# Optimization experiments

Hardware: AMD Instinct MI355X
Metric: run time of the kernel (lower is better)

## Reference

```python
import jax, jax.numpy as jnp
import numpy as np

S = 1024      # MAX_SEQ_LEN
D_IN = 4096
H = 32        # num_heads
G = 8         # num_kv_groups
HD = 128      # head_dim
GS = H // G   # group_size


def _rope(t, cos, sin):
    # t: [heads, S, HD]; cos/sin: [S, HD]
    half = HD // 2
    t1, t2 = t[..., :half], t[..., half:]
    rotated = jnp.concatenate([-t2, t1], axis=-1)
    return t * cos[None] + rotated * sin[None]


def setup_inputs() -> dict:
    key = jax.random.key(0)
    ks = jax.random.split(key, 8)
    x = jax.random.normal(ks[0], (1, S, D_IN), dtype=jnp.float32)
    mask = jnp.triu(jnp.ones((S, S), dtype=bool), k=1)  # causal: True above diagonal
    # RoPE tables (standard llama frequencies)
    inv_freq = 1.0 / (10000.0 ** (jnp.arange(0, HD, 2, dtype=jnp.float32) / HD))
    angles = jnp.arange(S, dtype=jnp.float32)[:, None] * inv_freq[None, :]  # [S, HD/2]
    angles = jnp.concatenate([angles, angles], axis=-1)                     # [S, HD]
    cos, sin = jnp.cos(angles), jnp.sin(angles)
    sc = 0.02
    Wq = jax.random.normal(ks[1], (D_IN, H * HD), dtype=jnp.float32) * sc
    Wk = jax.random.normal(ks[2], (D_IN, G * HD), dtype=jnp.float32) * sc
    Wv = jax.random.normal(ks[3], (D_IN, G * HD), dtype=jnp.float32) * sc
    Wo = jax.random.normal(ks[4], (H * HD, D_IN), dtype=jnp.float32) * sc
    return {"x": x, "mask": mask, "cos": cos, "sin": sin,
            "Wq": Wq, "Wk": Wk, "Wv": Wv, "Wo": Wo}


def reference(x, mask, cos, sin, Wq, Wk, Wv, Wo):
    b, n_tok, _ = x.shape  # b == 1 (module squeezes dim 0)
    xs = x[0]                                        # [S, d_in]
    q = (xs @ Wq).reshape(n_tok, H, HD).transpose(1, 0, 2)   # [H, S, HD]
    k = (xs @ Wk).reshape(n_tok, G, HD).transpose(1, 0, 2)   # [G, S, HD]
    v = (xs @ Wv).reshape(n_tok, G, HD).transpose(1, 0, 2)   # [G, S, HD]
    q = _rope(q, cos, sin)
    k = _rope(k, cos, sin)
    # GQA expansion: repeat_interleave over head dim
    k = jnp.repeat(k, GS, axis=0)                    # [H, S, HD]
    v = jnp.repeat(v, GS, axis=0)
    scores = jnp.einsum('hsd,htd->hst', q, k)        # [H, S, S]
    scores = jnp.where(mask[None], -jnp.inf, scores) / jnp.sqrt(jnp.float32(HD))
    weights = jax.nn.softmax(scores, axis=-1)
    ctx = jnp.einsum('hst,htd->hsd', weights, v)     # [H, S, HD]
    ctx = ctx.transpose(1, 0, 2).reshape(n_tok, H * HD)
    out = ctx @ Wo                                   # [S, d_in]
    return out[None]                                 # [1, S, d_in]
```

## Files before the change

kernel.cpp:

```cpp
#include <hip/hip_runtime.h>
#include <hip/hip_bf16.h>

#define S_LEN 1024
#define DIN 4096
#define NH 32
#define NG 8
#define HD 128

typedef __bf16 bf16x8 __attribute__((ext_vector_type(8)));
typedef __bf16 bf16x4 __attribute__((ext_vector_type(4)));
typedef float f32x4 __attribute__((ext_vector_type(4)));

__device__ __forceinline__ void gload_lds16(const void* g, void* l) {
  __builtin_amdgcn_global_load_lds(
      (const __attribute__((address_space(1))) unsigned int*)g,
      (__attribute__((address_space(3))) unsigned int*)l, 16, 0, 0);
}

__device__ __forceinline__ unsigned pack2bf(float a, float b) {
  union { __bf16 h[2]; unsigned u; } x;
  x.h[0] = (__bf16)a; x.h[1] = (__bf16)b;
  return x.u;
}

__global__ __launch_bounds__(256) void k_prep(const float* __restrict__ x,
                                              const float* __restrict__ Wq,
                                              const float* __restrict__ Wk,
                                              const float* __restrict__ Wv,
                                              const float* __restrict__ Wo,
                                              __bf16* __restrict__ xb,
                                              __bf16* __restrict__ WqkvT,
                                              __bf16* __restrict__ WoT) {
  __shared__ unsigned t3[32 * 256];
  const int tid = threadIdx.x;
  int bid = blockIdx.x;
  if (bid < 4096) {
    int i = bid * 256 + tid;
    const float4 v = ((const float4*)x)[i];
    bf16x4 o;
    o.x = (__bf16)v.x; o.y = (__bf16)v.y; o.z = (__bf16)v.z; o.w = (__bf16)v.w;
    ((bf16x4*)xb)[i] = o;
    return;
  }
  bid -= 4096;
  const int nt = bid % 40, kt = bid / 40;
  const int k0 = kt * 64;
  const float* W; __bf16* WT; int N, nsrc0, nd0;
  if (nt < 16)       { W = Wq; WT = WqkvT; N = 4096; nsrc0 = nt * 256;        nd0 = nt * 256; }
  else if (nt < 20)  { W = Wk; WT = WqkvT; N = 1024; nsrc0 = (nt - 16) * 256; nd0 = 4096 + (nt - 16) * 256; }
  else if (nt < 24)  { W = Wv; WT = WqkvT; N = 1024; nsrc0 = (nt - 20) * 256; nd0 = 5120 + (nt - 20) * 256; }
  else               { W = Wo; WT = WoT;   N = 4096; nsrc0 = (nt - 24) * 256; nd0 = (nt - 24) * 256; }

#pragma unroll
  for (int p = 0; p < 8; ++p) {
    int s = p * 256 + tid;
    int kp = s >> 6;
    int nq = s & 63;
    const float* src = &W[(size_t)(k0 + 2 * kp) * N + nsrc0 + 4 * nq];
    const float4 a = *(const float4*)src;
    const float4 b = *(const float4*)(src + N);
    int cphys = nq ^ ((kp >> 1) & 7);
    uint4 d;
    d.x = pack2bf(a.x, b.x);
    d.y = pack2bf(a.y, b.y);
    d.z = pack2bf(a.z, b.z);
    d.w = pack2bf(a.w, b.w);
    *(uint4*)&t3[kp * 256 + cphys * 4] = d;
  }
  __syncthreads();

#pragma unroll
  for (int it = 0; it < 8; ++it) {
    int n = it * 32 + (tid >> 3);
    int u = tid & 7;
    int nq = n >> 2, j = n & 3;
    uint4 d;
    d.x = t3[(4 * u + 0) * 256 + ((nq ^ (((4 * u + 0) >> 1) & 7)) << 2) + j];
    d.y = t3[(4 * u + 1) * 256 + ((nq ^ (((4 * u + 1) >> 1) & 7)) << 2) + j];
    d.z = t3[(4 * u + 2) * 256 + ((nq ^ (((4 * u + 2) >> 1) & 7)) << 2) + j];
    d.w = t3[(4 * u + 3) * 256 + ((nq ^ (((4 * u + 3) >> 1) & 7)) << 2) + j];
    *(uint4*)&WT[(size_t)(nd0 + n) * DIN + k0 + 8 * u] = d;
  }
}

__global__ __launch_bounds__(256) void k_rope(__bf16* __restrict__ Q, __bf16* __restrict__ Kb,
                                              const float* __restrict__ cosT,
                                              const float* __restrict__ sinT) {
  int idx = blockIdx.x * 256 + threadIdx.x;
  int d = (idx & 15) * 4;
  int row = idx >> 4;
  __bf16* p; int s;
  if (row < S_LEN * NH) { p = Q + (size_t)row * HD; s = row >> 5; }
  else { int r = row - S_LEN * NH; p = Kb + (size_t)r * HD; s = r >> 3; }
  const float4 c = *(const float4*)&cosT[s * HD + d];
  const float4 sn = *(const float4*)&sinT[s * HD + d];
  bf16x4 a = *(const bf16x4*)&p[d];
  bf16x4 b = *(const bf16x4*)&p[d + 64];
  bf16x4 oa, ob;
  oa.x = (__bf16)((float)a.x * c.x - (float)b.x * sn.x);
  oa.y = (__bf16)((float)a.y * c.y - (float)b.y * sn.y);
  oa.z = (__bf16)((float)a.z * c.z - (float)b.z * sn.z);
  oa.w = (__bf16)((float)a.w * c.w - (float)b.w * sn.w);
  ob.x = (__bf16)((float)b.x * c.x + (float)a.x * sn.x);
  ob.y = (__bf16)((float)b.y * c.y + (float)a.y * sn.y);
  ob.z = (__bf16)((float)b.z * c.z + (float)a.z * sn.z);
  ob.w = (__bf16)((float)b.w * c.w + (float)a.w * sn.w);
  *(bf16x4*)&p[d] = oa;
  *(bf16x4*)&p[d + 64] = ob;
}

template <int MODE>
__global__ __launch_bounds__(256, 3) void k_gemm(const __bf16* __restrict__ A,
                                                 const __bf16* __restrict__ Bt,
                                                 float* __restrict__ C,
                                                 __bf16* __restrict__ Qb,
                                                 __bf16* __restrict__ Kb,
                                                 __bf16* __restrict__ Vt) {
  __shared__ __bf16 As[2][128 * 64];
  __shared__ __bf16 Bs[2][64 * 64];
  const int bm = blockIdx.y, bn = blockIdx.x;
  const int K = DIN, NT = K / 64;

  const int tid = threadIdx.x, w = tid >> 6;
  const int l = tid & 63, l15 = l & 15, g4 = l >> 4;

  const __bf16* Asrc = A + (size_t)(bm * 128) * K;
  const __bf16* Bsrc = Bt + (size_t)(bn * 64) * K;

  f32x4 acc[2][4];
#pragma unroll
  for (int i = 0; i < 2; ++i)
#pragma unroll
    for (int j = 0; j < 4; ++j)
#pragma unroll
      for (int r = 0; r < 4; ++r) acc[i][j][r] = 0.f;

  auto issueA = [&](int t, __bf16* dst) {
#pragma unroll
    for (int p = 0; p < 4; ++p) {
      int c = p * 256 + tid;
      int row = c >> 3, gc = (c & 7) ^ (row & 7);
      gload_lds16(Asrc + (size_t)row * K + t * 64 + gc * 8, dst + (p * 256 + w * 64) * 8);
    }
  };
  auto issueB = [&](int t, __bf16* dst) {
#pragma unroll
    for (int p = 0; p < 2; ++p) {
      int c = p * 256 + tid;
      int row = c >> 3, gc = (c & 7) ^ (row & 7);
      gload_lds16(Bsrc + (size_t)row * K + t * 64 + gc * 8, dst + (p * 256 + w * 64) * 8);
    }
  };
  auto compute = [&](const __bf16* Ab, const __bf16* Bb) {
    bf16x8 af[2][2], bfr[4][2];
#pragma unroll
    for (int i = 0; i < 2; ++i) {
      int m = w * 32 + i * 16 + l15;
#pragma unroll
      for (int kk = 0; kk < 2; ++kk)
        af[i][kk] = *(const bf16x8*)((const char*)Ab + m * 128 + (((kk * 4 + g4) ^ (m & 7)) << 4));
    }
#pragma unroll
    for (int j = 0; j < 4; ++j) {
      int n = j * 16 + l15;
#pragma unroll
      for (int kk = 0; kk < 2; ++kk)
        bfr[j][kk] = *(const bf16x8*)((const char*)Bb + n * 128 + (((kk * 4 + g4) ^ (n & 7)) << 4));
    }
#pragma unroll
    for (int kk = 0; kk < 2; ++kk)
#pragma unroll
      for (int i = 0; i < 2; ++i)
#pragma unroll
        for (int j = 0; j < 4; ++j)
          acc[i][j] = __builtin_amdgcn_mfma_f32_16x16x32_bf16(af[i][kk], bfr[j][kk], acc[i][j], 0, 0, 0);
  };

  issueA(0, As[0]); issueB(0, Bs[0]);
  __syncthreads();

  for (int t = 0; t < NT; t += 2) {
    issueA(t + 1, As[1]); issueB(t + 1, Bs[1]);
    compute(As[0], Bs[0]);
    __syncthreads();
    if (t + 2 < NT) { issueA(t + 2, As[0]); issueB(t + 2, Bs[0]); }
    compute(As[1], Bs[1]);
    __syncthreads();
  }

  if constexpr (MODE == 0) {
#pragma unroll
    for (int i = 0; i < 2; ++i)
#pragma unroll
      for (int j = 0; j < 4; ++j)
#pragma unroll
        for (int r = 0; r < 4; ++r) {
          size_t row = bm * 128 + w * 32 + i * 16 + g4 * 4 + r;
          size_t col = bn * 64 + j * 16 + l15;
          C[row * 4096 + col] = acc[i][j][r];
        }
  } else {
    const int nb0 = bn * 64;
    if (bn < 80) {
      __bf16* dst = (bn < 64) ? Qb : Kb;
      int ldc = (bn < 64) ? 4096 : 1024;
      int coff = (bn < 64) ? 0 : 4096;
#pragma unroll
      for (int i = 0; i < 2; ++i)
#pragma unroll
        for (int j = 0; j < 4; ++j)
#pragma unroll
          for (int r = 0; r < 4; ++r) {
            size_t row = bm * 128 + w * 32 + i * 16 + g4 * 4 + r;
            size_t col = nb0 - coff + j * 16 + l15;
            dst[row * ldc + col] = (__bf16)acc[i][j][r];
          }
    } else {
#pragma unroll
      for (int i = 0; i < 2; ++i)
#pragma unroll
        for (int j = 0; j < 4; ++j) {
          size_t n = nb0 - 5120 + j * 16 + l15;
          size_t m0 = bm * 128 + w * 32 + i * 16 + g4 * 4;
          bf16x4 v;
          v.x = (__bf16)acc[i][j][0]; v.y = (__bf16)acc[i][j][1];
          v.z = (__bf16)acc[i][j][2]; v.w = (__bf16)acc[i][j][3];
          *(bf16x4*)&Vt[n * 1024 + m0] = v;
        }
    }
  }
}

__global__ __launch_bounds__(256) void k_attn(const __bf16* __restrict__ Q,
                                              const __bf16* __restrict__ Kb,
                                              const __bf16* __restrict__ Vt,
                                              __bf16* __restrict__ ctx) {
  __shared__ __align__(16) char lds_raw[65536];
  __bf16* Ks = (__bf16*)lds_raw;
  __bf16* Vs = (__bf16*)(lds_raw + 32768);

  const int h = blockIdx.y, g = h >> 2;
  const int q0 = blockIdx.x * 64;
  const int tid = threadIdx.x, w = tid >> 6, l = tid & 63;
  const int l15 = l & 15, g4 = l >> 4;
  const float scale = 0.08838834764831845f;

  bf16x8 qf[4];
  const int qrow = q0 + w * 16 + l15;
#pragma unroll
  for (int ks = 0; ks < 4; ++ks)
    qf[ks] = *(const bf16x8*)&Q[(size_t)qrow * (NH * HD) + h * HD + ks * 32 + g4 * 8];

  f32x4 acc[8];
#pragma unroll
  for (int i = 0; i < 8; ++i)
#pragma unroll
    for (int r = 0; r < 4; ++r) acc[i][r] = 0.f;
  float m_run = -__builtin_inff(), l_run = 0.f;

  const int ntiles = (q0 + 64 + 127) >> 7;
  for (int kt = 0; kt < ntiles; ++kt) {
    const int kv0 = kt * 128;
#pragma unroll
    for (int p = 0; p < 8; ++p) {
      int c = p * 256 + tid;
      int row = c >> 4, cc = c & 15;
      gload_lds16(&Kb[(size_t)(kv0 + row) * (NG * HD) + g * HD + ((cc ^ (row & 7)) << 3)],
                  &Ks[(p * 256 + w * 64) * 8]);
      gload_lds16(&Vt[(size_t)(g * HD + row) * S_LEN + kv0 + ((cc ^ (row & 7)) << 3)],
                  &Vs[(p * 256 + w * 64) * 8]);
    }
    __syncthreads();

    float sreg[8][4];
    const bool need_mask = (kv0 + 127 > q0);
#pragma unroll
    for (int tf = 0; tf < 8; ++tf) {
      f32x4 sa;
#pragma unroll
      for (int r = 0; r < 4; ++r) sa[r] = 0.f;
      int t_loc = tf * 16 + l15;
#pragma unroll
      for (int ks = 0; ks < 4; ++ks) {
        bf16x8 kf = *(const bf16x8*)((const char*)Ks + t_loc * 256 + (((ks * 4 + g4) ^ (t_loc & 7)) << 4));
        sa = __builtin_amdgcn_mfma_f32_16x16x32_bf16(kf, qf[ks], sa, 0, 0, 0);
      }
#pragma unroll
      for (int r = 0; r < 4; ++r) {
        float v = sa[r] * scale;
        if (need_mask && (kv0 + tf * 16 + g4 * 4 + r) > qrow) v = -__builtin_inff();
        sreg[tf][r] = v;
      }
    }
    float mx = -__builtin_inff();
#pragma unroll
    for (int tf = 0; tf < 8; ++tf)
#pragma unroll
      for (int r = 0; r < 4; ++r) mx = fmaxf(mx, sreg[tf][r]);
    mx = fmaxf(mx, __shfl_xor(mx, 16));
    mx = fmaxf(mx, __shfl_xor(mx, 32));
    const float m_new = fmaxf(m_run, mx);
    const float alpha = __expf(m_run - m_new);
    float ssum = 0.f;
#pragma unroll
    for (int tf = 0; tf < 8; ++tf)
#pragma unroll
      for (int r = 0; r < 4; ++r) {
        sreg[tf][r] = __expf(sreg[tf][r] - m_new);
        ssum += sreg[tf][r];
      }
    ssum += __shfl_xor(ssum, 16);
    ssum += __shfl_xor(ssum, 32);
    l_run = l_run * alpha + ssum;
    m_run = m_new;
    float ar[4];
#pragma unroll
    for (int r = 0; r < 4; ++r) ar[r] = __shfl(alpha, g4 * 4 + r);
#pragma unroll
    for (int nf = 0; nf < 8; ++nf)
#pragma unroll
      for (int r = 0; r < 4; ++r) acc[nf][r] *= ar[r];

    __syncthreads();

    char* pb = lds_raw + w * 4096;
#pragma unroll
    for (int tf = 0; tf < 8; ++tf) {
      int chunkc = 2 * tf + (g4 >> 1);
      int addr = l15 * 256 + ((chunkc ^ (l15 & 7)) << 4) + ((g4 & 1) << 3);
      *(unsigned*)(pb + addr)     = pack2bf(sreg[tf][0], sreg[tf][1]);
      *(unsigned*)(pb + addr + 4) = pack2bf(sreg[tf][2], sreg[tf][3]);
    }
    asm volatile("s_waitcnt lgkmcnt(0)" ::: "memory");
    bf16x8 pf[4];
#pragma unroll
    for (int ks = 0; ks < 4; ++ks)
      pf[ks] = *(const bf16x8*)(pb + l15 * 256 + (((ks * 4 + g4) ^ (l15 & 7)) << 4));
#pragma unroll
    for (int nf = 0; nf < 8; ++nf) {
      int d_loc = nf * 16 + l15;
#pragma unroll
      for (int ks = 0; ks < 4; ++ks) {
        bf16x8 vf = *(const bf16x8*)((const char*)Vs + d_loc * 256 + (((ks * 4 + g4) ^ (d_loc & 7)) << 4));
        acc[nf] = __builtin_amdgcn_mfma_f32_16x16x32_bf16(pf[ks], vf, acc[nf], 0, 0, 0);
      }
    }
    __syncthreads();
  }
  float li[4];
#pragma unroll
  for (int r = 0; r < 4; ++r) li[r] = 1.f / __shfl(l_run, g4 * 4 + r);
#pragma unroll
  for (int nf = 0; nf < 8; ++nf)
#pragma unroll
    for (int r = 0; r < 4; ++r) {
      size_t row = q0 + w * 16 + g4 * 4 + r;
      size_t col = (size_t)h * HD + nf * 16 + l15;
      ctx[row * (NH * HD) + col] = (__bf16)(acc[nf][r] * li[r]);
    }
}

extern "C" void kernel_launch(void* const* d_in, const int* in_sizes, int n_in,
                              void* d_out, int out_size, void* d_ws, size_t ws_size,
                              hipStream_t stream) {
  const float* x    = (const float*)d_in[0];
  const float* cosT = (const float*)d_in[2];
  const float* sinT = (const float*)d_in[3];
  const float* Wq   = (const float*)d_in[4];
  const float* Wk   = (const float*)d_in[5];
  const float* Wv   = (const float*)d_in[6];
  const float* Wo   = (const float*)d_in[7];
  float* out = (float*)d_out;

  char* ws = (char*)d_ws;
  const size_t MB = 1u << 20;
  __bf16* xb    = (__bf16*)(ws + 0);
  __bf16* WqkvT = (__bf16*)(ws + 8 * MB);
  __bf16* WoT   = (__bf16*)(ws + 56 * MB);
  __bf16* Qb    = (__bf16*)(ws + 88 * MB);
  __bf16* Kbuf  = (__bf16*)(ws + 96 * MB);
  __bf16* Vtb   = (__bf16*)(ws + 98 * MB);
  __bf16* ctxb  = (__bf16*)(ws + 0);

  k_prep<<<4096 + 2560, 256, 0, stream>>>(x, Wq, Wk, Wv, Wo, xb, WqkvT, WoT);

  k_gemm<1><<<dim3(96, 8), 256, 0, stream>>>(xb, WqkvT, nullptr, Qb, Kbuf, Vtb);

  k_rope<<<2560, 256, 0, stream>>>(Qb, Kbuf, cosT, sinT);

  k_attn<<<dim3(16, 32), 256, 0, stream>>>(Qb, Kbuf, Vtb, ctxb);

  k_gemm<0><<<dim3(64, 8), 256, 0, stream>>>(ctxb, WoT, out, nullptr, nullptr, nullptr);
}
```

Measured before the change: 214.9 us.

## Pre-tile transposed weights into contiguous pre-swizzled 64x64 blocks for B loads

The weight-conversion kernel now writes the transposed bf16 weights as contiguous 64x64 tiles, with the XOR swizzle already applied, ordered by N-tile then K-tile. The GEMM's B loader then reads each K-step tile as one contiguous 8 KB chunk instead of 64 rows strided by the full K. This removes per-row address arithmetic and makes the B global loads fully sequential. It depends on the GEMM consuming the same tile order, which the new Bsrc and issueB indexing provide.

```diff
diff --git a/kernel.cpp b/kernel.cpp
--- a/kernel.cpp
+++ b/kernel.cpp
@@ -45,11 +45,11 @@
   bid -= 4096;
   const int nt = bid % 40, kt = bid / 40;
   const int k0 = kt * 64;
-  const float* W; __bf16* WT; int N, nsrc0, nd0;
-  if (nt < 16)       { W = Wq; WT = WqkvT; N = 4096; nsrc0 = nt * 256;        nd0 = nt * 256; }
-  else if (nt < 20)  { W = Wk; WT = WqkvT; N = 1024; nsrc0 = (nt - 16) * 256; nd0 = 4096 + (nt - 16) * 256; }
-  else if (nt < 24)  { W = Wv; WT = WqkvT; N = 1024; nsrc0 = (nt - 20) * 256; nd0 = 5120 + (nt - 20) * 256; }
-  else               { W = Wo; WT = WoT;   N = 4096; nsrc0 = (nt - 24) * 256; nd0 = (nt - 24) * 256; }
+  const float* W; __bf16* WT; int N, nsrc0, tn0;
+  if (nt < 16)       { W = Wq; WT = WqkvT; N = 4096; nsrc0 = nt * 256;        tn0 = nt * 4; }
+  else if (nt < 20)  { W = Wk; WT = WqkvT; N = 1024; nsrc0 = (nt - 16) * 256; tn0 = 64 + (nt - 16) * 4; }
+  else if (nt < 24)  { W = Wv; WT = WqkvT; N = 1024; nsrc0 = (nt - 20) * 256; tn0 = 80 + (nt - 20) * 4; }
+  else               { W = Wo; WT = WoT;   N = 4096; nsrc0 = (nt - 24) * 256; tn0 = (nt - 24) * 4; }
 
 #pragma unroll
   for (int p = 0; p < 8; ++p) {
@@ -71,15 +71,20 @@
 
 #pragma unroll
   for (int it = 0; it < 8; ++it) {
-    int n = it * 32 + (tid >> 3);
-    int u = tid & 7;
+    int slot = it * 256 + tid;
+    int ts = slot >> 9;
+    int c = slot & 511;
+    int row = c >> 3;
+    int lc = (c & 7) ^ (row & 7);
+    int n = ts * 64 + row;
     int nq = n >> 2, j = n & 3;
+    int kp0 = 4 * lc;
     uint4 d;
-    d.x = t3[(4 * u + 0) * 256 + ((nq ^ (((4 * u + 0) >> 1) & 7)) << 2) + j];
-    d.y = t3[(4 * u + 1) * 256 + ((nq ^ (((4 * u + 1) >> 1) & 7)) << 2) + j];
-    d.z = t3[(4 * u + 2) * 256 + ((nq ^ (((4 * u + 2) >> 1) & 7)) << 2) + j];
-    d.w = t3[(4 * u + 3) * 256 + ((nq ^ (((4 * u + 3) >> 1) & 7)) << 2) + j];
-    *(uint4*)&WT[(size_t)(nd0 + n) * DIN + k0 + 8 * u] = d;
+    d.x = t3[(kp0 + 0) * 256 + ((nq ^ (((kp0 + 0) >> 1) & 7)) << 2) + j];
+    d.y = t3[(kp0 + 1) * 256 + ((nq ^ (((kp0 + 1) >> 1) & 7)) << 2) + j];
+    d.z = t3[(kp0 + 2) * 256 + ((nq ^ (((kp0 + 2) >> 1) & 7)) << 2) + j];
+    d.w = t3[(kp0 + 3) * 256 + ((nq ^ (((kp0 + 3) >> 1) & 7)) << 2) + j];
+    *(uint4*)&WT[(((size_t)tn0 + ts) * 64 + kt) * 4096 + (size_t)c * 8] = d;
   }
 }
 
@@ -125,7 +130,7 @@
   const int l = tid & 63, l15 = l & 15, g4 = l >> 4;
 
   const __bf16* Asrc = A + (size_t)(bm * 128) * K;
-  const __bf16* Bsrc = Bt + (size_t)(bn * 64) * K;
+  const __bf16* Bsrc = Bt + (size_t)bn * 64 * 4096;
 
   f32x4 acc[2][4];
 #pragma unroll
@@ -144,11 +149,11 @@
     }
   };
   auto issueB = [&](int t, __bf16* dst) {
+    const __bf16* tile = Bsrc + (size_t)t * 4096;
 #pragma unroll
     for (int p = 0; p < 2; ++p) {
       int c = p * 256 + tid;
-      int row = c >> 3, gc = (c & 7) ^ (row & 7);
-      gload_lds16(Bsrc + (size_t)row * K + t * 64 + gc * 8, dst + (p * 256 + w * 64) * 8);
+      gload_lds16(tile + (size_t)c * 8, dst + (p * 256 + w * 64) * 8);
     }
   };
   auto compute = [&](const __bf16* Ab, const __bf16* Bb) {
```

New measurement: 212.1 us. Within noise of the previous version (-1.3%).
